# Kernel optimization log

Measured on AMD Instinct MI355X. Metric: run time of the kernel, lower is better.

Reference implementation:

```python
import jax, jax.numpy as jnp
import numpy as np

EPS = 1e-6
SIGMA = 0.1  # temperature for pseudo-LBS blend weights


def _quat_rotate(q, v):
    # q: [..., 4] (w, x, y, z) unit quaternions, v: [..., 3]
    qw, qv = q[..., :1], q[..., 1:]
    t = 2.0 * jnp.cross(qv, v)
    return v + qw * t + jnp.cross(qv, t)


def _pairwise_sqdist(a, b):
    # a: [n, d], b: [m, d] -> [n, m]
    return (jnp.sum(a * a, -1, keepdims=True)
            + jnp.sum(b * b, -1)[None, :]
            - 2.0 * (a @ b.T))


def setup_inputs() -> dict:
    N, K, F, V, J, P, M, H = 300000, 80, 64, 6890, 24, 64, 64, 128
    key = jax.random.key(0)
    ks = jax.random.split(key, 16)
    s = lambda i, shape: jax.random.normal(ks[i], shape, dtype=jnp.float32) * 0.05
    return {
        "xyz": jax.random.normal(ks[0], (N, 3), dtype=jnp.float32),
        "feature": jax.random.normal(ks[1], (N, F), dtype=jnp.float32),
        "centers": jax.random.normal(ks[2], (K, F), dtype=jnp.float32),
        "smpl_verts": jax.random.normal(ks[3], (V, 3), dtype=jnp.float32),
        "skinning_weights": jax.random.uniform(ks[4], (V, J), dtype=jnp.float32),
        "body_pose_feature": jax.random.normal(ks[5], (J, P), dtype=jnp.float32),
        "w_body": s(6, (P + F, M)),
        "b_body": jnp.zeros((M,), jnp.float32),
        "w_pos1": s(7, (3 + M, H)),
        "b_pos1": jnp.zeros((H,), jnp.float32),
        "w_pos2": s(8, (H, M)),
        "b_pos2": jnp.zeros((M,), jnp.float32),
        "w_rot": s(9, (M, 4)),
        "b_rot": jnp.zeros((4,), jnp.float32),
        "w_trans": s(10, (M, 3)),
        "b_trans": jnp.zeros((3,), jnp.float32),
    }


def reference(xyz, feature, centers, smpl_verts, skinning_weights,
              body_pose_feature, w_body, b_body, w_pos1, b_pos1,
              w_pos2, b_pos2, w_rot, b_rot, w_trans, b_trans):
    # ---- soft k-means: soft assignment of N points to K garment joints ----
    a = jax.nn.softmax(-_pairwise_sqdist(feature, centers), axis=-1)  # [N, K]
    cnt = a.sum(axis=0) + EPS                                          # [K]
    # weighted segment-reduce: c_assign^T @ xyz, diag(1/count) normalize
    joint_xyz = (a.T @ xyz) / cnt[:, None]      # [K, 3]
    joint_feat = (a.T @ feature) / cnt[:, None]  # [K, F] (cluster centers)

    # ---- KNN (k=1) skin-weight lookup against SMPL canonical verts ----
    idx = jnp.argmin(_pairwise_sqdist(joint_xyz, smpl_verts), axis=-1)  # [K]
    pts_W = skinning_weights[idx]                                        # [K, J]

    # ---- garment pose decoder ----
    body_feat = pts_W @ body_pose_feature                 # [K, P]
    g = jnp.concatenate([body_feat, joint_feat], axis=-1)  # [K, P+F]
    g = jax.nn.gelu(g @ w_body + b_body)                   # [K, M]
    lo, hi = smpl_verts.min(0), smpl_verts.max(0)
    xn = 2.0 * (joint_xyz - lo) / (hi - lo + EPS) - 1.0    # aabb sym-normalize
    h = jax.nn.relu(jnp.concatenate([xn, g], -1) @ w_pos1 + b_pos1)
    g2 = h @ w_pos2 + b_pos2                               # [K, M]
    q = g2 @ w_rot + b_rot
    q = q / (jnp.linalg.norm(q, axis=-1, keepdims=True) + EPS)  # [K, 4]
    t = g2 @ w_trans + b_trans                                   # [K, 3]

    # ---- pseudo-LBS: blend per-joint transforms back to N points ----
    w = jax.nn.softmax(-_pairwise_sqdist(xyz, joint_xyz) / SIGMA, axis=-1)  # [N, K]
    qb = w @ q
    qb = qb / (jnp.linalg.norm(qb, axis=-1, keepdims=True) + EPS)  # [N, 4]
    deformed_xyz = _quat_rotate(qb, xyz) + w @ t                    # [N, 3]
    return deformed_xyz
```

## Files before the change

### kernel.cpp

```cpp
#include <hip/hip_runtime.h>
#include <math.h>

#define N_PTS 300000
#define NJ 80
#define FDIM 64
#define VN 6890
#define NROUND 9375
#define GRID_A 512
#define WAVES_A (GRID_A * 4)

typedef __attribute__((ext_vector_type(8))) short short8;
typedef __attribute__((ext_vector_type(4))) float f32x4;

union Frag { uint32_t u[4]; short8 v; };

__device__ __forceinline__ uint32_t packhi(float a, float b) {
  return (__float_as_uint(a) >> 16) | (__float_as_uint(b) & 0xFFFF0000u);
}
__device__ __forceinline__ uint32_t packlo(float a, float b) {
  float la = a - __uint_as_float(__float_as_uint(a) & 0xFFFF0000u);
  float lb = b - __uint_as_float(__float_as_uint(b) & 0xFFFF0000u);
  return packhi(la, lb);
}

#define DPPF(x, ctrl) __uint_as_float((uint32_t)__builtin_amdgcn_update_dpp( \
    0, (int)__float_as_uint(x), (ctrl), 0xF, 0xF, true))

__global__ __launch_bounds__(256, 2) void kA(
    const float* __restrict__ xyz, const float* __restrict__ feature,
    const float* __restrict__ centers, float* __restrict__ jacc,
    float* __restrict__ part)
{
  __shared__ ushort sClo[NJ][72];
  __shared__ ushort sT[4][NJ][36];

  const int tid = threadIdx.x;
  const int w = tid >> 6;
  const int l = tid & 63;
  const int i = l & 15;
  const int g = l >> 4;

  for (int idx = tid; idx < 4 * NJ * 36; idx += 256) ((ushort*)sT)[idx] = 0;
  for (int idx = tid; idx < NJ * FDIM; idx += 256) {
    float f = centers[idx];
    float lo = f - __uint_as_float(__float_as_uint(f) & 0xFFFF0000u);
    sClo[idx >> 6][idx & 63] = (ushort)(__float_as_uint(lo) >> 16);
  }

  Frag bh[5][2];
  float cn[5];
#pragma unroll
  for (int nt = 0; nt < 5; ++nt) {
    float s = 0.f;
#pragma unroll
    for (int ks = 0; ks < 2; ++ks) {
      const float4* cp = (const float4*)(centers + (size_t)(i + 16*nt) * FDIM + 32*ks + 8*g);
      float4 v0 = cp[0], v1 = cp[1];
      bh[nt][ks].u[0] = packhi(v0.x, v0.y);
      bh[nt][ks].u[1] = packhi(v0.z, v0.w);
      bh[nt][ks].u[2] = packhi(v1.x, v1.y);
      bh[nt][ks].u[3] = packhi(v1.z, v1.w);
      s += v0.x*v0.x + v0.y*v0.y + v0.z*v0.z + v0.w*v0.w
         + v1.x*v1.x + v1.y*v1.y + v1.z*v1.z + v1.w*v1.w;
    }
    s += __shfl_xor(s, 16);
    s += __shfl_xor(s, 32);
    cn[nt] = s;
  }

  f32x4 acc2[5][5];
#pragma unroll
  for (int a = 0; a < 5; ++a)
#pragma unroll
    for (int b = 0; b < 5; ++b) acc2[a][b] = (f32x4){0.f, 0.f, 0.f, 0.f};

  __syncthreads();

  const int gw = blockIdx.x * 4 + w;
  for (int rd = gw; rd < NROUND; rd += WAVES_A) {
    const int pbase = rd * 32;

    float4 vv[2][2][2];
    float  xq[2];
#pragma unroll
    for (int c = 0; c < 2; ++c) {
      const int pt = pbase + 16*c + i;
#pragma unroll
      for (int ks = 0; ks < 2; ++ks) {
        const float4* fp = (const float4*)(feature + (size_t)pt * FDIM + 32*ks + 8*g);
        vv[c][ks][0] = fp[0];
        vv[c][ks][1] = fp[1];
      }
      xq[c] = (g < 3) ? xyz[(size_t)pt * 3 + g] : 1.0f;
    }

    Frag pA[5];
#pragma unroll
    for (int c = 0; c < 2; ++c) {
      f32x4 acc1[5];
#pragma unroll
      for (int nt = 0; nt < 5; ++nt) acc1[nt] = (f32x4){0.f, 0.f, 0.f, 0.f};

#pragma unroll
      for (int ks = 0; ks < 2; ++ks) {
        float4 v0 = vv[c][ks][0], v1 = vv[c][ks][1];
        Frag ah, al;
        ah.u[0] = packhi(v0.x, v0.y); ah.u[1] = packhi(v0.z, v0.w);
        ah.u[2] = packhi(v1.x, v1.y); ah.u[3] = packhi(v1.z, v1.w);
        al.u[0] = packlo(v0.x, v0.y); al.u[1] = packlo(v0.z, v0.w);
        al.u[2] = packlo(v1.x, v1.y); al.u[3] = packlo(v1.z, v1.w);
        const int d0 = 32*ks + 8*g, pcol = 16*c + i;
        sT[w][d0+0][pcol] = (ushort)(ah.u[0] & 0xFFFFu);
        sT[w][d0+1][pcol] = (ushort)(ah.u[0] >> 16);
        sT[w][d0+2][pcol] = (ushort)(ah.u[1] & 0xFFFFu);
        sT[w][d0+3][pcol] = (ushort)(ah.u[1] >> 16);
        sT[w][d0+4][pcol] = (ushort)(ah.u[2] & 0xFFFFu);
        sT[w][d0+5][pcol] = (ushort)(ah.u[2] >> 16);
        sT[w][d0+6][pcol] = (ushort)(ah.u[3] & 0xFFFFu);
        sT[w][d0+7][pcol] = (ushort)(ah.u[3] >> 16);
#pragma unroll
        for (int nt = 0; nt < 5; ++nt) {
          Frag bl;
          *(uint4*)bl.u = *(const uint4*)&sClo[i + 16*nt][32*ks + 8*g];
          acc1[nt] = __builtin_amdgcn_mfma_f32_16x16x32_bf16(ah.v, bh[nt][ks].v, acc1[nt], 0, 0, 0);
          acc1[nt] = __builtin_amdgcn_mfma_f32_16x16x32_bf16(al.v, bh[nt][ks].v, acc1[nt], 0, 0, 0);
          acc1[nt] = __builtin_amdgcn_mfma_f32_16x16x32_bf16(ah.v, bl.v,        acc1[nt], 0, 0, 0);
        }
      }
      sT[w][64 + g][16*c + i] =
          (g < 3) ? (ushort)(__float_as_uint(xq[c]) >> 16) : (ushort)0x3F80;

      f32x4 e5[5];
#pragma unroll
      for (int nt = 0; nt < 5; ++nt) {
#pragma unroll
        for (int r = 0; r < 4; ++r) e5[nt][r] = 2.f * acc1[nt][r] - cn[nt];
      }
      float rs[4];
#pragma unroll
      for (int r = 0; r < 4; ++r) {
        float m = e5[0][r];
#pragma unroll
        for (int nt = 1; nt < 5; ++nt) m = fmaxf(m, e5[nt][r]);
        m = fmaxf(m, DPPF(m, 0xB1));
        m = fmaxf(m, DPPF(m, 0x4E));
        m = fmaxf(m, DPPF(m, 0x141));
        m = fmaxf(m, DPPF(m, 0x140));
        float s = 0.f;
#pragma unroll
        for (int nt = 0; nt < 5; ++nt) {
          float e = __expf(e5[nt][r] - m);
          e5[nt][r] = e;
          s += e;
        }
        s += DPPF(s, 0xB1);
        s += DPPF(s, 0x4E);
        s += DPPF(s, 0x141);
        s += DPPF(s, 0x140);
        rs[r] = __builtin_amdgcn_rcpf(s);
      }
#pragma unroll
      for (int nt = 0; nt < 5; ++nt) {
        pA[nt].u[2*c + 0] = packhi(e5[nt][0] * rs[0], e5[nt][1] * rs[1]);
        pA[nt].u[2*c + 1] = packhi(e5[nt][2] * rs[2], e5[nt][3] * rs[3]);
      }
    }

#pragma unroll
    for (int ct = 0; ct < 5; ++ct) {
      Frag B;
      *(uint2*)&B.u[0] = *(const uint2*)&sT[w][16*ct + i][4*g];
      *(uint2*)&B.u[2] = *(const uint2*)&sT[w][16*ct + i][16 + 4*g];
#pragma unroll
      for (int nt = 0; nt < 5; ++nt)
        acc2[nt][ct] = __builtin_amdgcn_mfma_f32_16x16x32_bf16(pA[nt].v, B.v, acc2[nt][ct], 0, 0, 0);
    }
  }

  __syncthreads();
  float* sJ = (float*)&sT[0][0][0];
  for (int idx = tid; idx < 5440; idx += 256) sJ[idx] = 0.f;
  __syncthreads();
#pragma unroll
  for (int ww = 0; ww < 4; ++ww) {
    if (w == ww) {
#pragma unroll
      for (int nt = 0; nt < 5; ++nt)
#pragma unroll
        for (int ct = 0; ct < 5; ++ct) {
          if (ct < 4 || i < 4) {
            const int col = 16*ct + i;
#pragma unroll
            for (int r = 0; r < 4; ++r)
              sJ[(16*nt + 4*g + r) * 68 + col] += acc2[nt][ct][r];
          }
        }
    }
    __syncthreads();
  }
  if (part) {
    for (int idx = tid; idx < 5440; idx += 256)
      part[(size_t)blockIdx.x * 5440 + idx] = sJ[idx];
  } else {
    for (int idx = tid; idx < 5440; idx += 256)
      atomicAdd(&jacc[idx], sJ[idx]);
  }
}

__global__ __launch_bounds__(256) void kR(const float* __restrict__ part,
                                          float* __restrict__ jacc)
{
  const int bx = blockIdx.x;
  const int cg = bx % 22, sl = bx / 22;
  const int t = cg * 256 + threadIdx.x;
  if (t >= 5440) return;
  const int b0 = sl * 32;
  float s0 = 0.f, s1 = 0.f, s2 = 0.f, s3 = 0.f;
  for (int b = b0; b < b0 + 32; b += 4) {
    s0 += part[(size_t)(b+0) * 5440 + t];
    s1 += part[(size_t)(b+1) * 5440 + t];
    s2 += part[(size_t)(b+2) * 5440 + t];
    s3 += part[(size_t)(b+3) * 5440 + t];
  }
  atomicAdd(&jacc[t], (s0 + s1) + (s2 + s3));
}

__global__ __launch_bounds__(64) void kB(
    const float* __restrict__ jacc, const float* __restrict__ smpl,
    const float* __restrict__ sw, const float* __restrict__ bpf,
    const float* __restrict__ w_body, const float* __restrict__ b_body,
    const float* __restrict__ w_pos1, const float* __restrict__ b_pos1,
    const float* __restrict__ w_pos2, const float* __restrict__ b_pos2,
    const float* __restrict__ w_rot,  const float* __restrict__ b_rot,
    const float* __restrict__ w_trans,const float* __restrict__ b_trans,
    float* __restrict__ jpack, float* __restrict__ qpack,
    float* __restrict__ tpack)
{
  const int k = blockIdx.x;
  const int l = threadIdx.x;
  __shared__ float gin[128];
  __shared__ float in2[67];
  __shared__ float h2[128];
  __shared__ float g2[64];
  __shared__ float q7[8];

  const float cnt = jacc[k*68 + 67] + 1e-6f;
  gin[64 + l] = jacc[k*68 + l] / cnt;
  const float jx = jacc[k*68 + 64] / cnt;
  const float jy = jacc[k*68 + 65] / cnt;
  const float jz = jacc[k*68 + 66] / cnt;

  float lo0 = 1e30f, lo1 = 1e30f, lo2 = 1e30f;
  float hi0 = -1e30f, hi1 = -1e30f, hi2 = -1e30f;
  float best = 1e30f; int bi = 0;
  for (int v = l; v < VN; v += 64) {
    float x = smpl[v*3], y = smpl[v*3+1], z = smpl[v*3+2];
    lo0 = fminf(lo0, x); hi0 = fmaxf(hi0, x);
    lo1 = fminf(lo1, y); hi1 = fmaxf(hi1, y);
    lo2 = fminf(lo2, z); hi2 = fmaxf(hi2, z);
    float dx = x - jx, dy = y - jy, dz = z - jz;
    float d = dx*dx + dy*dy + dz*dz;
    if (d < best) { best = d; bi = v; }
  }
#pragma unroll
  for (int m = 1; m < 64; m <<= 1) {
    lo0 = fminf(lo0, __shfl_xor(lo0, m));
    lo1 = fminf(lo1, __shfl_xor(lo1, m));
    lo2 = fminf(lo2, __shfl_xor(lo2, m));
    hi0 = fmaxf(hi0, __shfl_xor(hi0, m));
    hi1 = fmaxf(hi1, __shfl_xor(hi1, m));
    hi2 = fmaxf(hi2, __shfl_xor(hi2, m));
    float d2 = __shfl_xor(best, m); int i2 = __shfl_xor(bi, m);
    if (d2 < best || (d2 == best && i2 < bi)) { best = d2; bi = i2; }
  }

  {
    float s = 0.f;
    for (int j = 0; j < 24; ++j) s += sw[bi*24 + j] * bpf[j*64 + l];
    gin[l] = s;
  }
  if (l < 3) {
    float lo = (l == 0) ? lo0 : (l == 1) ? lo1 : lo2;
    float hi = (l == 0) ? hi0 : (l == 1) ? hi1 : hi2;
    float jc = (l == 0) ? jx : (l == 1) ? jy : jz;
    in2[l] = 2.f * (jc - lo) / (hi - lo + 1e-6f) - 1.f;
  }
  __syncthreads();

  {
    float s = b_body[l];
    for (int t = 0; t < 128; ++t) s += gin[t] * w_body[t*64 + l];
    float u = 0.7978845608028654f * (s + 0.044715f * s * s * s);
    float e = __expf(2.f * u);
    float th = 1.f - 2.f / (e + 1.f);
    in2[3 + l] = 0.5f * s * (1.f + th);
  }
  __syncthreads();

#pragma unroll
  for (int half = 0; half < 2; ++half) {
    const int m = l + 64*half;
    float s = b_pos1[m];
    for (int t = 0; t < 67; ++t) s += in2[t] * w_pos1[t*128 + m];
    h2[m] = fmaxf(s, 0.f);
  }
  __syncthreads();

  {
    float s = b_pos2[l];
    for (int t = 0; t < 128; ++t) s += h2[t] * w_pos2[t*64 + l];
    g2[l] = s;
  }
  __syncthreads();

  if (l < 4) {
    float s = b_rot[l];
    for (int t = 0; t < 64; ++t) s += g2[t] * w_rot[t*4 + l];
    q7[l] = s;
  } else if (l < 7) {
    const int j = l - 4;
    float s = b_trans[j];
    for (int t = 0; t < 64; ++t) s += g2[t] * w_trans[t*3 + j];
    q7[l] = s;
  }
  __syncthreads();
  if (l == 0) {
    float q0 = q7[0], q1 = q7[1], q2 = q7[2], q3 = q7[3];
    float rn = 1.f / (sqrtf(q0*q0 + q1*q1 + q2*q2 + q3*q3) + 1e-6f);
    *(float4*)&qpack[k*4] = make_float4(q0*rn, q1*rn, q2*rn, q3*rn);
    *(float4*)&tpack[k*4] = make_float4(q7[4], q7[5], q7[6], 0.f);
    *(float4*)&jpack[k*4] = make_float4(jx, jy, jz, jx*jx + jy*jy + jz*jz);
  }
}

__global__ __launch_bounds__(256) void kC(
    const float* __restrict__ xyz, const float* __restrict__ jpack,
    const float* __restrict__ qpack, const float* __restrict__ tpack,
    float* __restrict__ out)
{
  __shared__ float4 sj[NJ], sq[NJ], st[NJ];
  const int tid = threadIdx.x;
  if (tid < 80)        sj[tid]       = ((const float4*)jpack)[tid];
  else if (tid < 160)  sq[tid - 80]  = ((const float4*)qpack)[tid - 80];
  else if (tid < 240)  st[tid - 160] = ((const float4*)tpack)[tid - 160];
  __syncthreads();

  const int p = blockIdx.x * 256 + tid;
  if (p >= N_PTS) return;

  float x0 = xyz[p*3], x1 = xyz[p*3+1], x2 = xyz[p*3+2];
  float lv[NJ];
  float m = -1e30f;
#pragma unroll
  for (int k = 0; k < NJ; ++k) {
    float4 j = sj[k];
    lv[k] = (2.f*(x0*j.x + x1*j.y + x2*j.z) - j.w) * 10.0f;
    m = fmaxf(m, lv[k]);
  }
  float s = 0.f;
  float qb0=0,qb1=0,qb2=0,qb3=0, tb0=0,tb1=0,tb2=0;
#pragma unroll
  for (int k = 0; k < NJ; ++k) {
    float e = __expf(lv[k] - m);
    s += e;
    float4 q = sq[k];
    float4 t = st[k];
    qb0 += e*q.x; qb1 += e*q.y; qb2 += e*q.z; qb3 += e*q.w;
    tb0 += e*t.x; tb1 += e*t.y; tb2 += e*t.z;
  }
  float rs = 1.f / s;
  qb0*=rs; qb1*=rs; qb2*=rs; qb3*=rs; tb0*=rs; tb1*=rs; tb2*=rs;
  float nrm = sqrtf(qb0*qb0+qb1*qb1+qb2*qb2+qb3*qb3) + 1e-6f;
  float rn = 1.f / nrm;
  float qw = qb0*rn, qx = qb1*rn, qy = qb2*rn, qz = qb3*rn;
  float t2x = 2.f*(qy*x2 - qz*x1);
  float t2y = 2.f*(qz*x0 - qx*x2);
  float t2z = 2.f*(qx*x1 - qy*x0);
  float cx = qy*t2z - qz*t2y;
  float cy = qz*t2x - qx*t2z;
  float cz = qx*t2y - qy*t2x;
  out[p*3]   = x0 + qw*t2x + cx + tb0;
  out[p*3+1] = x1 + qw*t2y + cy + tb1;
  out[p*3+2] = x2 + qw*t2z + cz + tb2;
}

extern "C" void kernel_launch(void* const* d_in, const int* in_sizes, int n_in,
                              void* d_out, int out_size, void* d_ws, size_t ws_size,
                              hipStream_t stream) {
  const float* xyz     = (const float*)d_in[0];
  const float* feature = (const float*)d_in[1];
  const float* centers = (const float*)d_in[2];
  const float* smpl    = (const float*)d_in[3];
  const float* sw      = (const float*)d_in[4];
  const float* bpf     = (const float*)d_in[5];
  const float* w_body  = (const float*)d_in[6];
  const float* b_body  = (const float*)d_in[7];
  const float* w_pos1  = (const float*)d_in[8];
  const float* b_pos1  = (const float*)d_in[9];
  const float* w_pos2  = (const float*)d_in[10];
  const float* b_pos2  = (const float*)d_in[11];
  const float* w_rot   = (const float*)d_in[12];
  const float* b_rot   = (const float*)d_in[13];
  const float* w_trans = (const float*)d_in[14];
  const float* b_trans = (const float*)d_in[15];
  float* out = (float*)d_out;

  float* ws    = (float*)d_ws;
  float* jacc  = ws;
  float* jpack = ws + 5440;
  float* qpack = ws + 5760;
  float* tpack = ws + 6080;
  float* part  = ws + 6400;

  const size_t need = (size_t)6400 + (size_t)GRID_A * 5440;
  const bool use_part = (ws_size / 4) >= need;
  float* part_arg = use_part ? part : nullptr;

  hipMemsetAsync(jacc, 0, 5440 * sizeof(float), stream);
  kA<<<dim3(GRID_A), dim3(256), 0, stream>>>(xyz, feature, centers, jacc, part_arg);
  if (use_part)
    kR<<<dim3(22 * 16), dim3(256), 0, stream>>>(part, jacc);
  kB<<<dim3(NJ), dim3(64), 0, stream>>>(jacc, smpl, sw, bpf,
                                        w_body, b_body, w_pos1, b_pos1,
                                        w_pos2, b_pos2, w_rot, b_rot,
                                        w_trans, b_trans, jpack, qpack, tpack);
  kC<<<dim3((N_PTS + 255) / 256), dim3(256), 0, stream>>>(xyz, jpack, qpack, tpack, out);
}
```

Baseline: 135.5 us.

## Prefetch next round's features in kA, double grid, coalesce kC xyz I/O via LDS

The k-means accumulation kernel now loads the next round's feature and xyz registers before running the current round's MFMAs, so global load latency can overlap with compute. The grid is doubled to 1024 blocks, and the partial-sum reduction kernel is adjusted to match. The LBS kernel stages xyz loads and output stores through shared memory so global accesses are coalesced instead of stride-3. The costs are more register pressure from the prefetch buffers and the separated acc1 arrays, a larger partial buffer to reduce, and extra barriers in kC.

```diff
diff --git a/kernel.cpp b/kernel.cpp
--- a/kernel.cpp
+++ b/kernel.cpp
@@ -6,7 +6,7 @@
 #define FDIM 64
 #define VN 6890
 #define NROUND 9375
-#define GRID_A 512
+#define GRID_A 1024
 #define WAVES_A (GRID_A * 4)
 
 typedef __attribute__((ext_vector_type(8))) short short8;
@@ -76,65 +76,81 @@
 
   __syncthreads();
 
-  const int gw = blockIdx.x * 4 + w;
-  for (int rd = gw; rd < NROUND; rd += WAVES_A) {
-    const int pbase = rd * 32;
-
-    float4 vv[2][2][2];
-    float  xq[2];
+  float4 vv[2][2][2];
+  float  xq[2];
+
+#define LOADR(RD) do {                                                        \
+    const int pb_ = (RD) * 32;                                                \
+    _Pragma("unroll")                                                         \
+    for (int c_ = 0; c_ < 2; ++c_) {                                          \
+      const int pt_ = pb_ + 16*c_ + i;                                        \
+      const float4* f0_ = (const float4*)(feature + (size_t)pt_ * FDIM + 8*g);\
+      vv[c_][0][0] = f0_[0]; vv[c_][0][1] = f0_[1];                           \
+      const float4* f1_ = (const float4*)(feature + (size_t)pt_ * FDIM + 32 + 8*g);\
+      vv[c_][1][0] = f1_[0]; vv[c_][1][1] = f1_[1];                           \
+      xq[c_] = (g < 3) ? xyz[(size_t)pt_ * 3 + g] : 1.0f;                     \
+    }                                                                         \
+  } while (0)
+
+  int rd = blockIdx.x * 4 + w;
+  if (rd < NROUND) LOADR(rd);
+
+  while (rd < NROUND) {
+    Frag fh[2][2], fl[2][2];
 #pragma unroll
     for (int c = 0; c < 2; ++c) {
-      const int pt = pbase + 16*c + i;
-#pragma unroll
-      for (int ks = 0; ks < 2; ++ks) {
-        const float4* fp = (const float4*)(feature + (size_t)pt * FDIM + 32*ks + 8*g);
-        vv[c][ks][0] = fp[0];
-        vv[c][ks][1] = fp[1];
-      }
-      xq[c] = (g < 3) ? xyz[(size_t)pt * 3 + g] : 1.0f;
-    }
-
-    Frag pA[5];
-#pragma unroll
-    for (int c = 0; c < 2; ++c) {
-      f32x4 acc1[5];
-#pragma unroll
-      for (int nt = 0; nt < 5; ++nt) acc1[nt] = (f32x4){0.f, 0.f, 0.f, 0.f};
-
 #pragma unroll
       for (int ks = 0; ks < 2; ++ks) {
         float4 v0 = vv[c][ks][0], v1 = vv[c][ks][1];
-        Frag ah, al;
-        ah.u[0] = packhi(v0.x, v0.y); ah.u[1] = packhi(v0.z, v0.w);
-        ah.u[2] = packhi(v1.x, v1.y); ah.u[3] = packhi(v1.z, v1.w);
-        al.u[0] = packlo(v0.x, v0.y); al.u[1] = packlo(v0.z, v0.w);
-        al.u[2] = packlo(v1.x, v1.y); al.u[3] = packlo(v1.z, v1.w);
+        fh[c][ks].u[0] = packhi(v0.x, v0.y); fh[c][ks].u[1] = packhi(v0.z, v0.w);
+        fh[c][ks].u[2] = packhi(v1.x, v1.y); fh[c][ks].u[3] = packhi(v1.z, v1.w);
+        fl[c][ks].u[0] = packlo(v0.x, v0.y); fl[c][ks].u[1] = packlo(v0.z, v0.w);
+        fl[c][ks].u[2] = packlo(v1.x, v1.y); fl[c][ks].u[3] = packlo(v1.z, v1.w);
         const int d0 = 32*ks + 8*g, pcol = 16*c + i;
-        sT[w][d0+0][pcol] = (ushort)(ah.u[0] & 0xFFFFu);
-        sT[w][d0+1][pcol] = (ushort)(ah.u[0] >> 16);
-        sT[w][d0+2][pcol] = (ushort)(ah.u[1] & 0xFFFFu);
-        sT[w][d0+3][pcol] = (ushort)(ah.u[1] >> 16);
-        sT[w][d0+4][pcol] = (ushort)(ah.u[2] & 0xFFFFu);
-        sT[w][d0+5][pcol] = (ushort)(ah.u[2] >> 16);
-        sT[w][d0+6][pcol] = (ushort)(ah.u[3] & 0xFFFFu);
-        sT[w][d0+7][pcol] = (ushort)(ah.u[3] >> 16);
+        sT[w][d0+0][pcol] = (ushort)(fh[c][ks].u[0] & 0xFFFFu);
+        sT[w][d0+1][pcol] = (ushort)(fh[c][ks].u[0] >> 16);
+        sT[w][d0+2][pcol] = (ushort)(fh[c][ks].u[1] & 0xFFFFu);
+        sT[w][d0+3][pcol] = (ushort)(fh[c][ks].u[1] >> 16);
+        sT[w][d0+4][pcol] = (ushort)(fh[c][ks].u[2] & 0xFFFFu);
+        sT[w][d0+5][pcol] = (ushort)(fh[c][ks].u[2] >> 16);
+        sT[w][d0+6][pcol] = (ushort)(fh[c][ks].u[3] & 0xFFFFu);
+        sT[w][d0+7][pcol] = (ushort)(fh[c][ks].u[3] >> 16);
+      }
+      sT[w][64 + g][16*c + i] =
+          (g < 3) ? (ushort)(__float_as_uint(xq[c]) >> 16) : (ushort)0x3F80;
+    }
+
+    const int rdn = rd + WAVES_A;
+    if (rdn < NROUND) LOADR(rdn);
+
+    f32x4 acc1[2][5];
+#pragma unroll
+    for (int c = 0; c < 2; ++c)
+#pragma unroll
+      for (int nt = 0; nt < 5; ++nt) acc1[c][nt] = (f32x4){0.f, 0.f, 0.f, 0.f};
+
+#pragma unroll
+    for (int c = 0; c < 2; ++c)
+#pragma unroll
+      for (int ks = 0; ks < 2; ++ks) {
 #pragma unroll
         for (int nt = 0; nt < 5; ++nt) {
           Frag bl;
           *(uint4*)bl.u = *(const uint4*)&sClo[i + 16*nt][32*ks + 8*g];
-          acc1[nt] = __builtin_amdgcn_mfma_f32_16x16x32_bf16(ah.v, bh[nt][ks].v, acc1[nt], 0, 0, 0);
-          acc1[nt] = __builtin_amdgcn_mfma_f32_16x16x32_bf16(al.v, bh[nt][ks].v, acc1[nt], 0, 0, 0);
-          acc1[nt] = __builtin_amdgcn_mfma_f32_16x16x32_bf16(ah.v, bl.v,        acc1[nt], 0, 0, 0);
+          acc1[c][nt] = __builtin_amdgcn_mfma_f32_16x16x32_bf16(fh[c][ks].v, bh[nt][ks].v, acc1[c][nt], 0, 0, 0);
+          acc1[c][nt] = __builtin_amdgcn_mfma_f32_16x16x32_bf16(fl[c][ks].v, bh[nt][ks].v, acc1[c][nt], 0, 0, 0);
+          acc1[c][nt] = __builtin_amdgcn_mfma_f32_16x16x32_bf16(fh[c][ks].v, bl.v,         acc1[c][nt], 0, 0, 0);
         }
       }
-      sT[w][64 + g][16*c + i] =
-          (g < 3) ? (ushort)(__float_as_uint(xq[c]) >> 16) : (ushort)0x3F80;
-
+
+    Frag pA[5];
+#pragma unroll
+    for (int c = 0; c < 2; ++c) {
       f32x4 e5[5];
 #pragma unroll
       for (int nt = 0; nt < 5; ++nt) {
 #pragma unroll
-        for (int r = 0; r < 4; ++r) e5[nt][r] = 2.f * acc1[nt][r] - cn[nt];
+        for (int r = 0; r < 4; ++r) e5[nt][r] = 2.f * acc1[c][nt][r] - cn[nt];
       }
       float rs[4];
 #pragma unroll
@@ -175,6 +191,7 @@
       for (int nt = 0; nt < 5; ++nt)
         acc2[nt][ct] = __builtin_amdgcn_mfma_f32_16x16x32_bf16(pA[nt].v, B.v, acc2[nt][ct], 0, 0, 0);
     }
+    rd = rdn;
   }
 
   __syncthreads();
@@ -205,6 +222,7 @@
     for (int idx = tid; idx < 5440; idx += 256)
       atomicAdd(&jacc[idx], sJ[idx]);
   }
+#undef LOADR
 }
 
 __global__ __launch_bounds__(256) void kR(const float* __restrict__ part,
@@ -214,9 +232,9 @@
   const int cg = bx % 22, sl = bx / 22;
   const int t = cg * 256 + threadIdx.x;
   if (t >= 5440) return;
-  const int b0 = sl * 32;
+  const int b0 = sl * (GRID_A / 16);
   float s0 = 0.f, s1 = 0.f, s2 = 0.f, s3 = 0.f;
-  for (int b = b0; b < b0 + 32; b += 4) {
+  for (int b = b0; b < b0 + GRID_A / 16; b += 4) {
     s0 += part[(size_t)(b+0) * 5440 + t];
     s1 += part[(size_t)(b+1) * 5440 + t];
     s2 += part[(size_t)(b+2) * 5440 + t];
@@ -339,16 +357,23 @@
     float* __restrict__ out)
 {
   __shared__ float4 sj[NJ], sq[NJ], st[NJ];
+  __shared__ float sxy[768];
   const int tid = threadIdx.x;
+  const int pbase = blockIdx.x * 256;
+  const int nval = min(256, N_PTS - pbase);
+  const int cnt3 = nval * 3;
+
   if (tid < 80)        sj[tid]       = ((const float4*)jpack)[tid];
   else if (tid < 160)  sq[tid - 80]  = ((const float4*)qpack)[tid - 80];
   else if (tid < 240)  st[tid - 160] = ((const float4*)tpack)[tid - 160];
-  __syncthreads();
-
-  const int p = blockIdx.x * 256 + tid;
-  if (p >= N_PTS) return;
-
-  float x0 = xyz[p*3], x1 = xyz[p*3+1], x2 = xyz[p*3+2];
+  for (int t = tid; t < cnt3; t += 256) sxy[t] = xyz[(size_t)pbase * 3 + t];
+  __syncthreads();
+
+  const bool valid = tid < nval;
+  float x0 = 0.f, x1 = 0.f, x2 = 0.f;
+  if (valid) { x0 = sxy[tid*3]; x1 = sxy[tid*3+1]; x2 = sxy[tid*3+2]; }
+  __syncthreads();
+
   float lv[NJ];
   float m = -1e30f;
 #pragma unroll
@@ -379,9 +404,13 @@
   float cx = qy*t2z - qz*t2y;
   float cy = qz*t2x - qx*t2z;
   float cz = qx*t2y - qy*t2x;
-  out[p*3]   = x0 + qw*t2x + cx + tb0;
-  out[p*3+1] = x1 + qw*t2y + cy + tb1;
-  out[p*3+2] = x2 + qw*t2z + cz + tb2;
+  float r0 = x0 + qw*t2x + cx + tb0;
+  float r1 = x1 + qw*t2y + cy + tb1;
+  float r2 = x2 + qw*t2z + cz + tb2;
+
+  if (valid) { sxy[tid*3] = r0; sxy[tid*3+1] = r1; sxy[tid*3+2] = r2; }
+  __syncthreads();
+  for (int t = tid; t < cnt3; t += 256) out[(size_t)pbase * 3 + t] = sxy[t];
 }
 
 extern "C" void kernel_launch(void* const* d_in, const int* in_sizes, int n_in,
```

After: 192.0 us. +41.7%, slower.

## Raise kA grid and occupancy, coalesce kC xyz I/O through LDS

Applied to the files above, without the earlier changes.

Raises the kA grid from 512 to 1172 blocks and the launch-bounds minimum from 2 to 3 blocks per SM to fill more of the GPU, and changes the kR partial reduction to cover the larger block count with 74-block slices. kC now stages the strided xyz loads and output stores through shared memory so global accesses are coalesced. The risks are register pressure and spills in kA under the tighter bound, and more partial buffers to write and reduce.

```diff
diff --git a/kernel.cpp b/kernel.cpp
--- a/kernel.cpp
+++ b/kernel.cpp
@@ -6,7 +6,7 @@
 #define FDIM 64
 #define VN 6890
 #define NROUND 9375
-#define GRID_A 512
+#define GRID_A 1172
 #define WAVES_A (GRID_A * 4)
 
 typedef __attribute__((ext_vector_type(8))) short short8;
@@ -26,7 +26,7 @@
 #define DPPF(x, ctrl) __uint_as_float((uint32_t)__builtin_amdgcn_update_dpp( \
     0, (int)__float_as_uint(x), (ctrl), 0xF, 0xF, true))
 
-__global__ __launch_bounds__(256, 2) void kA(
+__global__ __launch_bounds__(256, 3) void kA(
     const float* __restrict__ xyz, const float* __restrict__ feature,
     const float* __restrict__ centers, float* __restrict__ jacc,
     float* __restrict__ part)
@@ -214,15 +214,16 @@
   const int cg = bx % 22, sl = bx / 22;
   const int t = cg * 256 + threadIdx.x;
   if (t >= 5440) return;
-  const int b0 = sl * 32;
-  float s0 = 0.f, s1 = 0.f, s2 = 0.f, s3 = 0.f;
-  for (int b = b0; b < b0 + 32; b += 4) {
-    s0 += part[(size_t)(b+0) * 5440 + t];
-    s1 += part[(size_t)(b+1) * 5440 + t];
-    s2 += part[(size_t)(b+2) * 5440 + t];
-    s3 += part[(size_t)(b+3) * 5440 + t];
-  }
-  atomicAdd(&jacc[t], (s0 + s1) + (s2 + s3));
+  const int b0 = sl * 74;
+  const int b1 = min(GRID_A, b0 + 74);
+  float s0 = 0.f, s1 = 0.f;
+  int b = b0;
+  for (; b + 1 < b1; b += 2) {
+    s0 += part[(size_t)(b + 0) * 5440 + t];
+    s1 += part[(size_t)(b + 1) * 5440 + t];
+  }
+  if (b < b1) s0 += part[(size_t)b * 5440 + t];
+  atomicAdd(&jacc[t], s0 + s1);
 }
 
 __global__ __launch_bounds__(64) void kB(
@@ -339,16 +340,23 @@
     float* __restrict__ out)
 {
   __shared__ float4 sj[NJ], sq[NJ], st[NJ];
+  __shared__ float sxy[768];
   const int tid = threadIdx.x;
+  const int pbase = blockIdx.x * 256;
+  const int nval = min(256, N_PTS - pbase);
+  const int cnt3 = nval * 3;
+
   if (tid < 80)        sj[tid]       = ((const float4*)jpack)[tid];
   else if (tid < 160)  sq[tid - 80]  = ((const float4*)qpack)[tid - 80];
   else if (tid < 240)  st[tid - 160] = ((const float4*)tpack)[tid - 160];
-  __syncthreads();
-
-  const int p = blockIdx.x * 256 + tid;
-  if (p >= N_PTS) return;
-
-  float x0 = xyz[p*3], x1 = xyz[p*3+1], x2 = xyz[p*3+2];
+  for (int t = tid; t < cnt3; t += 256) sxy[t] = xyz[(size_t)pbase * 3 + t];
+  __syncthreads();
+
+  const bool valid = tid < nval;
+  float x0 = 0.f, x1 = 0.f, x2 = 0.f;
+  if (valid) { x0 = sxy[tid*3]; x1 = sxy[tid*3+1]; x2 = sxy[tid*3+2]; }
+  __syncthreads();
+
   float lv[NJ];
   float m = -1e30f;
 #pragma unroll
@@ -379,9 +387,13 @@
   float cx = qy*t2z - qz*t2y;
   float cy = qz*t2x - qx*t2z;
   float cz = qx*t2y - qy*t2x;
-  out[p*3]   = x0 + qw*t2x + cx + tb0;
-  out[p*3+1] = x1 + qw*t2y + cy + tb1;
-  out[p*3+2] = x2 + qw*t2z + cz + tb2;
+  float r0 = x0 + qw*t2x + cx + tb0;
+  float r1 = x1 + qw*t2y + cy + tb1;
+  float r2 = x2 + qw*t2z + cz + tb2;
+
+  if (valid) { sxy[tid*3] = r0; sxy[tid*3+1] = r1; sxy[tid*3+2] = r2; }
+  __syncthreads();
+  for (int t = tid; t < cnt3; t += 256) out[(size_t)pbase * 3 + t] = sxy[t];
 }
 
 extern "C" void kernel_launch(void* const* d_in, const int* in_sizes, int n_in,
```

After: 288.1 us. 113% more time.
